# Kernel optimization log

Hardware: AMD Instinct MI355X
Metric: run time of the kernel (lower is better)

## Reference

```python
import jax, jax.numpy as jnp
import numpy as np

B, N, F_IN = 4, 8000, 3          # batch, electrons per event, (x,y,z) features
HID, S, T = 128, 1024, 1024      # MLP hidden, n_sensors, waveform_ticks
INV_SQRT_2PI = 0.3989422804


def _mlp(x, W1, b1, W2, b2):
    h = jax.nn.relu(x @ W1 + b1)
    return h @ W2 + b2


def setup_inputs() -> dict:
    key = jax.random.key(0)
    ks = jax.random.split(key, 12)
    simulator_input = jax.random.normal(ks[0], (B, N, F_IN), dtype=jnp.float32)
    # z positions in tick units, spread across the waveform
    z_positions = jax.random.uniform(ks[1], (B, N), dtype=jnp.float32) * (T - 1)
    mask = jnp.ones((B, N, 1), dtype=jnp.float32)
    s1 = 1.0 / np.sqrt(F_IN)
    s2 = 1.0 / np.sqrt(HID)
    Wp1 = jax.random.normal(ks[2], (F_IN, HID), dtype=jnp.float32) * s1
    bp1 = jnp.zeros((HID,), dtype=jnp.float32)
    Wp2 = jax.random.normal(ks[3], (HID, S), dtype=jnp.float32) * s2
    bp2 = jnp.zeros((S,), dtype=jnp.float32)
    Wa1 = jax.random.normal(ks[4], (F_IN, HID), dtype=jnp.float32) * s1
    ba1 = jnp.zeros((HID,), dtype=jnp.float32)
    Wa2 = jax.random.normal(ks[5], (HID, S), dtype=jnp.float32) * s2
    ba2 = jnp.zeros((S,), dtype=jnp.float32)
    nn_bin_sigma = 5.0 * jnp.ones((1,), dtype=jnp.float32)  # self.variable init
    return dict(simulator_input=simulator_input, z_positions=z_positions, mask=mask,
                Wp1=Wp1, bp1=bp1, Wp2=Wp2, bp2=bp2,
                Wa1=Wa1, ba1=ba1, Wa2=Wa2, ba2=ba2,
                nn_bin_sigma=nn_bin_sigma)


def reference(simulator_input, z_positions, mask,
              Wp1, bp1, Wp2, bp2, Wa1, ba1, Wa2, ba2, nn_bin_sigma):
    # sensor response per electron: sigmoid(prob MLP) * amp MLP * mask  -> [B,N,S]
    sensor_probs = jax.nn.sigmoid(_mlp(simulator_input, Wp1, bp1, Wp2, bp2))
    el_light_amp = _mlp(simulator_input, Wa1, ba1, Wa2, ba2)
    response_of_sensors = el_light_amp * sensor_probs * mask

    # Gaussian binning kernel over waveform ticks: [B,N,T]
    ticks = jnp.arange(T, dtype=simulator_input.dtype)          # linspace(0, T-1, T)
    sigma = nn_bin_sigma[0]
    diff = ticks[None, None, :] - z_positions[:, :, None]
    exp_values = jnp.exp(-(diff ** 2) / (2.0 * sigma ** 2)) * (INV_SQRT_2PI / jnp.sqrt(sigma ** 2))

    # per-batch waveforms = sensor_response.T @ exp_values -> [B,S,T]; then sum over batch
    waveforms = jnp.einsum('bns,bnt->st', response_of_sensors, exp_values)
    return waveforms  # [S, T]
```

## Files before the change

### kernel.cpp

```cpp
#include <hip/hip_runtime.h>


#define BN_E   32000
#define NBLK   125
#define HIDW   128
#define S_DIM  1024
#define T_DIM  1024
#define NBKT   16
#define KSPL   4
#define MAXPAD (BN_E + NBKT * 31)
#define MAXCG  ((MAXPAD + 31) / 32)
#define INV_SQRT_2PI 0.3989422804f

typedef __attribute__((ext_vector_type(8))) unsigned short u16x8;
typedef __attribute__((ext_vector_type(8))) __bf16         bf16x8;
typedef __attribute__((ext_vector_type(4))) float          f32x4;

static __device__ __forceinline__ unsigned short f2bf(float f) {
    union { float f; unsigned int u; } v; v.f = f;
    unsigned int r = v.u + 0x7FFFu + ((v.u >> 16) & 1u);
    return (unsigned short)(r >> 16);
}

static __device__ __forceinline__ f32x4 mfma16(u16x8 a, u16x8 b, f32x4 c) {
    return __builtin_amdgcn_mfma_f32_16x16x32_bf16(
        __builtin_bit_cast(bf16x8, a), __builtin_bit_cast(bf16x8, b), c, 0, 0, 0);
}

static __device__ __forceinline__ int bucket_of(float z) {
    int b = (int)floorf((z - 31.f) * (1.f / 64.f));
    return min(max(b, 0), NBKT - 1);
}

__global__ __launch_bounds__(256) void k_count(const float* __restrict__ z,
                                               int* __restrict__ bc,
                                               float* __restrict__ out) {
    int bx = blockIdx.x;
    if (bx >= NBLK) {
        int idx = (bx - NBLK) * 256 + threadIdx.x;
        ((f32x4*)out)[idx] = (f32x4){0.f, 0.f, 0.f, 0.f};
        return;
    }
    __shared__ int h[NBKT];
    if (threadIdx.x < NBKT) h[threadIdx.x] = 0;
    __syncthreads();
    int e = bx * 256 + threadIdx.x;
    atomicAdd(&h[bucket_of(z[e])], 1);
    __syncthreads();
    if (threadIdx.x < NBKT) bc[bx * NBKT + threadIdx.x] = h[threadIdx.x];
}

__global__ __launch_bounds__(256) void k_fillscan(const float* __restrict__ z,
                                                  const int* __restrict__ bc,
                                                  int* __restrict__ meta,
                                                  int* __restrict__ list) {
    __shared__ int part[16][16];
    __shared__ int segoff[16][16];
    __shared__ int cntL[NBKT], pstartL[NBKT], baseL[NBKT], h[NBKT];
    int t = threadIdx.x, b = t & 15, seg = t >> 4;
    int v[8]; int sum = 0;
#pragma unroll
    for (int i = 0; i < 8; ++i) {
        int blk = seg * 8 + i;
        v[i] = (blk < NBLK) ? bc[blk * NBKT + b] : 0;
        sum += v[i];
    }
    part[seg][b] = sum;
    if (t < NBKT) h[t] = 0;
    __syncthreads();
    if (t < NBKT) {
        int run = 0;
        for (int s = 0; s < 16; ++s) { segoff[s][t] = run; run += part[s][t]; }
        cntL[t] = run;
    }
    __syncthreads();
    if (t == 0) {
        int s = 0;
        for (int i = 0; i < NBKT; ++i) {
            pstartL[i] = s;
            s += ((cntL[i] + 31) >> 5) << 5;
        }
        if (blockIdx.x == 0) {
            for (int i = 0; i < NBKT; ++i) { meta[i] = cntL[i]; meta[32 + i] = pstartL[i]; }
            meta[48] = s;
        }
    }
    __syncthreads();
    if (t < NBKT) {
        int me = blockIdx.x;
        int run = segoff[me >> 3][t];
        for (int k = 0; k < (me & 7); ++k)
            run += bc[((me >> 3) * 8 + k) * NBKT + t];
        baseL[t] = pstartL[t] + run;
    }
    __syncthreads();
    int e = blockIdx.x * 256 + t;
    int b2 = bucket_of(z[e]);
    int r = atomicAdd(&h[b2], 1);
    list[baseL[b2] + r] = e;
}

__global__ __launch_bounds__(256) void k_prep(
    const float* __restrict__ x, const float* __restrict__ zg,
    const float* __restrict__ maskg, const float* __restrict__ sigp,
    const float* __restrict__ Wp1, const float* __restrict__ bp1,
    const float* __restrict__ Wa1, const float* __restrict__ ba1,
    const float* __restrict__ Wp2, const float* __restrict__ Wa2,
    const int* __restrict__ meta, const int* __restrict__ list,
    unsigned short* __restrict__ HpS, unsigned short* __restrict__ HaS,
    unsigned short* __restrict__ GT,
    unsigned short* __restrict__ WfP, unsigned short* __restrict__ WfA) {
    int bx = blockIdx.x;
    if (bx < MAXCG) {
        int tid = threadIdx.x;

        __shared__ float W1L[1024];
        __shared__ float zzL[32], cmL[32];
        __shared__ int metaL[33];
        if (tid < 33) metaL[tid] = meta[tid < 16 ? tid : (tid < 32 ? tid + 16 : 48)];
        if (tid < 96)                        ((float4*)W1L)[tid]              = ((const float4*)Wp1)[tid];
        else if (tid < 128)                  ((float4*)(W1L + 384))[tid - 96] = ((const float4*)bp1)[tid - 96];
        else if (tid < 224)                  ((float4*)(W1L + 512))[tid - 128]= ((const float4*)Wa1)[tid - 128];
        else                                 ((float4*)(W1L + 896))[tid - 224]= ((const float4*)ba1)[tid - 224];
        __syncthreads();

        int pos0 = bx * 32;
        if (pos0 >= metaL[32]) return;
        int b = 15;
        while (metaL[16 + b] > pos0) --b;
        int tb = b * 64, cnt = metaL[b], pstart = metaL[16 + b];

        if (tid < 32) {
            int pos = pos0 + tid;
            bool real = (pos - pstart) < cnt;
            int ev = real ? list[pos] : 0;
            float sigma = sigp[0];
            zzL[tid] = real ? zg[ev] : 0.f;
            cmL[tid] = real ? (INV_SQRT_2PI / sigma) * maskg[ev] : 0.f;
        }

        {
            int e_l = tid & 31, part = tid >> 5;
            int pos = pos0 + e_l;
            bool real = (pos - pstart) < cnt;
            int ev = real ? list[pos] : 0;
            float x0 = 0.f, x1 = 0.f, x2 = 0.f;
            if (real) { x0 = x[ev * 3]; x1 = x[ev * 3 + 1]; x2 = x[ev * 3 + 2]; }
            unsigned short hp[16], ha[16];
#pragma unroll
            for (int i = 0; i < 16; ++i) {
                int j = part * 16 + i;
                float hv = x0 * W1L[j] + x1 * W1L[128 + j] + x2 * W1L[256 + j] + W1L[384 + j];
                float av = x0 * W1L[512 + j] + x1 * W1L[640 + j] + x2 * W1L[768 + j] + W1L[896 + j];
                hp[i] = real ? f2bf(fmaxf(hv, 0.f)) : (unsigned short)0;
                ha[i] = real ? f2bf(fmaxf(av, 0.f)) : (unsigned short)0;
            }
#pragma unroll
            for (int h2 = 0; h2 < 2; ++h2) {
                int u = (2 * part + h2) * 32 + e_l;
                *(uint4*)&HpS[(size_t)bx * 4096 + u * 8] = ((uint4*)hp)[h2];
                *(uint4*)&HaS[(size_t)bx * 4096 + u * 8] = ((uint4*)ha)[h2];
            }
        }
        __syncthreads();

        {
            float sigma = sigp[0];
            float nis2 = -1.f / (2.f * sigma * sigma);
#pragma unroll
            for (int uu = 0; uu < 2; ++uu) {
                int u = tid * 2 + uu;
                int n8 = u >> 6, q = (u >> 4) & 3, c = u & 15;
                float tt = (float)(tb + n8 * 16 + c);
                unsigned short g8[8];
#pragma unroll
                for (int j = 0; j < 8; ++j) {
                    int e = q * 8 + j;
                    float d = tt - zzL[e];
                    g8[j] = f2bf(cmL[e] * __expf(d * d * nis2));
                }
                *(uint4*)&GT[(size_t)bx * 4096 + u * 8] = *(uint4*)g8;
            }
        }
    } else {
        int bid = bx - MAXCG;
        const float* src = (bid & 64) ? Wa2 : Wp2;
        unsigned short* dst = (bid & 64) ? WfA : WfP;
        int rem = bid & 63;
        int kq = rem >> 2;
        int s  = (rem & 3) * 256 + threadIdx.x;
        int ks = kq >> 2, q = kq & 3;
        unsigned short fr[8];
#pragma unroll
        for (int j = 0; j < 8; ++j)
            fr[j] = f2bf(src[(ks * 32 + q * 8 + j) * S_DIM + s]);
        ((u16x8*)dst)[kq * S_DIM + s] = *(u16x8*)fr;
    }
}

__global__ __launch_bounds__(512, 4) void k_main(
    const unsigned short* __restrict__ HpS, const unsigned short* __restrict__ HaS,
    const unsigned short* __restrict__ WfP, const unsigned short* __restrict__ WfA,
    const float* __restrict__ bp2, const float* __restrict__ ba2,
    const int* __restrict__ meta, const unsigned short* __restrict__ GT,
    float* __restrict__ out) {

    const int bk     = blockIdx.x / KSPL;
    const int kspl   = blockIdx.x % KSPL;
    const int s0     = blockIdx.y * 128;
    const int tb     = bk * 64;
    const int cnt    = meta[bk];
    const int pstart = meta[32 + bk];
    const int nch    = (cnt + 31) >> 5;
    const int per    = (nch + KSPL - 1) / KSPL;
    const int c0     = kspl * per;
    const int c1     = min(nch, c0 + per);
    if (c0 >= c1) return;

    const int tid = threadIdx.x;
    const int w = tid >> 6, l = tid & 63, q = l >> 4, c = l & 15;

    __shared__ __align__(16) uint4 HpL[1024];
    __shared__ __align__(16) uint4 HaL[1024];
    __shared__ __align__(16) unsigned short RspL[128 * 40];

    const u16x8* WfPv = (const u16x8*)WfP;
    const u16x8* WfAv = (const u16x8*)WfA;
    const int sg = s0 + w * 16 + c;
    u16x8 wP[4], wA[4];
#pragma unroll
    for (int ks = 0; ks < 4; ++ks) {
        wP[ks] = WfPv[(ks * 4 + q) * S_DIM + sg];
        wA[ks] = WfAv[(ks * 4 + q) * S_DIM + sg];
    }
    const float bp2v = bp2[sg];
    const float ba2v = ba2[sg];

    const f32x4 z4 = { 0.f, 0.f, 0.f, 0.f };
    f32x4 acc2[8];
#pragma unroll
    for (int n8 = 0; n8 < 8; ++n8) acc2[n8] = z4;

    const uint4* Hp4 = (const uint4*)HpS;
    const uint4* Ha4 = (const uint4*)HaS;
    const int cgBase = pstart >> 5;

    size_t cb = (size_t)(cgBase + c0) * 512;
    uint4 p = Hp4[cb + tid];
    uint4 a = Ha4[cb + tid];

    for (int ci = c0; ci < c1; ++ci) {
        const int buf = ((ci - c0) & 1) << 9;
        HpL[buf + tid] = p;
        HaL[buf + tid] = a;

        int nc = min(ci + 1, c1 - 1);
        cb = (size_t)(cgBase + nc) * 512;
        p = Hp4[cb + tid];
        a = Ha4[cb + tid];
        __syncthreads();

        const unsigned short* gt = GT + (size_t)(cgBase + ci) * 4096;
        u16x8 bfr[8];
#pragma unroll
        for (int n8 = 0; n8 < 8; ++n8)
            bfr[n8] = *(const u16x8*)&gt[((n8 * 4 + q) * 16 + c) * 8];

        const u16x8* StHp = (const u16x8*)(HpL + buf);
        const u16x8* StHa = (const u16x8*)(HaL + buf);
        f32x4 aP[2], aA[2];
        aP[0] = z4; aP[1] = z4; aA[0] = z4; aA[1] = z4;
#pragma unroll
        for (int ks = 0; ks < 4; ++ks) {
            u16x8 hp0 = StHp[(ks * 4 + q) * 32 + c];
            u16x8 hp1 = StHp[(ks * 4 + q) * 32 + c + 16];
            u16x8 ha0 = StHa[(ks * 4 + q) * 32 + c];
            u16x8 ha1 = StHa[(ks * 4 + q) * 32 + c + 16];
            aP[0] = mfma16(hp0, wP[ks], aP[0]);
            aP[1] = mfma16(hp1, wP[ks], aP[1]);
            aA[0] = mfma16(ha0, wA[ks], aA[0]);
            aA[1] = mfma16(ha1, wA[ks], aA[1]);
        }

#pragma unroll
        for (int m = 0; m < 2; ++m) {
            f32x4 pp = aP[m], aa = aA[m];
            unsigned long long pk = 0;
#pragma unroll
            for (int r = 0; r < 4; ++r) {
                float pr = pp[r] + bp2v;
                float ar = aa[r] + ba2v;
                float sg2 = __builtin_amdgcn_rcpf(1.f + __expf(-pr));
                pk |= (unsigned long long)f2bf(sg2 * ar) << (16 * r);
            }
            *(unsigned long long*)&RspL[(w * 16 + c) * 40 + m * 16 + q * 4] = pk;
        }

        u16x8 afr = *(const u16x8*)&RspL[(w * 16 + c) * 40 + q * 8];
#pragma unroll
        for (int n8 = 0; n8 < 8; ++n8)
            acc2[n8] = mfma16(afr, bfr[n8], acc2[n8]);
    }

#pragma unroll
    for (int n8 = 0; n8 < 8; ++n8) {
        int t = tb + n8 * 16 + c;
        if (t < T_DIM) {
            int srow = s0 + w * 16 + q * 4;
#pragma unroll
            for (int r = 0; r < 4; ++r)
                atomicAdd(&out[(srow + r) * T_DIM + t], acc2[n8][r]);
        }
    }
}


extern "C" void kernel_launch(void* const* d_in, const int* in_sizes, int n_in,
                              void* d_out, int out_size, void* d_ws, size_t ws_size,
                              hipStream_t stream) {
    const float* x    = (const float*)d_in[0];
    const float* zp   = (const float*)d_in[1];
    const float* mask = (const float*)d_in[2];
    const float* Wp1  = (const float*)d_in[3];
    const float* bp1  = (const float*)d_in[4];
    const float* Wp2  = (const float*)d_in[5];
    const float* bp2  = (const float*)d_in[6];
    const float* Wa1  = (const float*)d_in[7];
    const float* ba1  = (const float*)d_in[8];
    const float* Wa2  = (const float*)d_in[9];
    const float* ba2  = (const float*)d_in[10];
    const float* sig  = (const float*)d_in[11];

    char* ws = (char*)d_ws;
    unsigned short* HpS  = (unsigned short*)(ws);
    unsigned short* HaS  = (unsigned short*)(ws + 8323072);
    unsigned short* WfP  = (unsigned short*)(ws + 16646144);
    unsigned short* WfA  = (unsigned short*)(ws + 16908288);
    int*            meta = (int*)(ws + 17170432);
    int*            list = (int*)(ws + 17170688);
    int*            bc   = (int*)(ws + 17300736);
    unsigned short* GT   = (unsigned short*)(ws + 17308736);

    k_count<<<NBLK + 1024, 256, 0, stream>>>(zp, bc, (float*)d_out);
    k_fillscan<<<NBLK, 256, 0, stream>>>(zp, bc, meta, list);
    k_prep<<<MAXCG + 128, 256, 0, stream>>>(x, zp, mask, sig,
                                            Wp1, bp1, Wa1, ba1, Wp2, Wa2,
                                            meta, list, HpS, HaS, GT, WfP, WfA);
    k_main<<<dim3(NBKT * KSPL, 8, 1), 512, 0, stream>>>(
        HpS, HaS, WfP, WfA, bp2, ba2, meta, GT, (float*)d_out);
}
```

Measured before the change: 148.7 us.

## Replace output atomics with per-block partial buffers and a deterministic reduce kernel

The main kernel no longer atomically adds its 128x128 tile (64 ticks of own bucket plus overlap into the next bucket) into the output. Each block instead writes its tile to a private partial buffer in workspace, zeroing it when the block has no work. A new reduce kernel sums the KSPL split partials and the overlapping neighbour bucket per output element. This removes atomic contention and the separate output-zeroing pass. In exchange it adds an extra kernel launch and roughly 16 MB of partial-buffer traffic.

```diff
diff --git a/kernel.cpp b/kernel.cpp
--- a/kernel.cpp
+++ b/kernel.cpp
@@ -33,14 +33,8 @@
 }
 
 __global__ __launch_bounds__(256) void k_count(const float* __restrict__ z,
-                                               int* __restrict__ bc,
-                                               float* __restrict__ out) {
+                                               int* __restrict__ bc) {
     int bx = blockIdx.x;
-    if (bx >= NBLK) {
-        int idx = (bx - NBLK) * 256 + threadIdx.x;
-        ((f32x4*)out)[idx] = (f32x4){0.f, 0.f, 0.f, 0.f};
-        return;
-    }
     __shared__ int h[NBKT];
     if (threadIdx.x < NBKT) h[threadIdx.x] = 0;
     __syncthreads();
@@ -203,22 +197,29 @@
     const unsigned short* __restrict__ WfP, const unsigned short* __restrict__ WfA,
     const float* __restrict__ bp2, const float* __restrict__ ba2,
     const int* __restrict__ meta, const unsigned short* __restrict__ GT,
-    float* __restrict__ out) {
+    float* __restrict__ P) {
 
     const int bk     = blockIdx.x / KSPL;
     const int kspl   = blockIdx.x % KSPL;
     const int s0     = blockIdx.y * 128;
-    const int tb     = bk * 64;
     const int cnt    = meta[bk];
     const int pstart = meta[32 + bk];
     const int nch    = (cnt + 31) >> 5;
     const int per    = (nch + KSPL - 1) / KSPL;
     const int c0     = kspl * per;
     const int c1     = min(nch, c0 + per);
-    if (c0 >= c1) return;
 
     const int tid = threadIdx.x;
     const int w = tid >> 6, l = tid & 63, q = l >> 4, c = l & 15;
+    const f32x4 z4 = { 0.f, 0.f, 0.f, 0.f };
+    float* Pp = P + (size_t)(blockIdx.x * 8 + blockIdx.y) * 16384;
+
+    if (c0 >= c1) {
+        f32x4* p4 = (f32x4*)Pp;
+#pragma unroll
+        for (int i = 0; i < 8; ++i) p4[i * 512 + tid] = z4;
+        return;
+    }
 
     __shared__ __align__(16) uint4 HpL[1024];
     __shared__ __align__(16) uint4 HaL[1024];
@@ -236,7 +237,6 @@
     const float bp2v = bp2[sg];
     const float ba2v = ba2[sg];
 
-    const f32x4 z4 = { 0.f, 0.f, 0.f, 0.f };
     f32x4 acc2[8];
 #pragma unroll
     for (int n8 = 0; n8 < 8; ++n8) acc2[n8] = z4;
@@ -304,14 +304,39 @@
 
 #pragma unroll
     for (int n8 = 0; n8 < 8; ++n8) {
-        int t = tb + n8 * 16 + c;
-        if (t < T_DIM) {
-            int srow = s0 + w * 16 + q * 4;
-#pragma unroll
-            for (int r = 0; r < 4; ++r)
-                atomicAdd(&out[(srow + r) * T_DIM + t], acc2[n8][r]);
-        }
-    }
+        int tl = n8 * 16 + c;
+        int sl = w * 16 + q * 4;
+#pragma unroll
+        for (int r = 0; r < 4; ++r)
+            Pp[(sl + r) * 128 + tl] = acc2[n8][r];
+    }
+}
+
+__global__ __launch_bounds__(256) void k_reduce(const float* __restrict__ P,
+                                                float* __restrict__ out) {
+    int idx = blockIdx.x * 256 + threadIdx.x;
+    int t0  = (idx & 255) << 2;
+    int s   = idx >> 8;
+    int bkA = t0 >> 6;
+    int colA = t0 & 63;
+    int y    = s >> 7;
+    int sl   = s & 127;
+    const f32x4* P4 = (const f32x4*)P;
+    f32x4 acc = { 0.f, 0.f, 0.f, 0.f };
+#pragma unroll
+    for (int k = 0; k < KSPL; ++k) {
+        f32x4 v = P4[((size_t)(bkA * KSPL + k) * 8 + y) * 4096 + sl * 32 + (colA >> 2)];
+        acc[0] += v[0]; acc[1] += v[1]; acc[2] += v[2]; acc[3] += v[3];
+    }
+    if (bkA > 0) {
+        int colB = 64 + colA;
+#pragma unroll
+        for (int k = 0; k < KSPL; ++k) {
+            f32x4 v = P4[((size_t)((bkA - 1) * KSPL + k) * 8 + y) * 4096 + sl * 32 + (colB >> 2)];
+            acc[0] += v[0]; acc[1] += v[1]; acc[2] += v[2]; acc[3] += v[3];
+        }
+    }
+    ((f32x4*)out)[idx] = acc;
 }
 
 
@@ -340,12 +365,14 @@
     int*            list = (int*)(ws + 17170688);
     int*            bc   = (int*)(ws + 17300736);
     unsigned short* GT   = (unsigned short*)(ws + 17308736);
-
-    k_count<<<NBLK + 1024, 256, 0, stream>>>(zp, bc, (float*)d_out);
+    float*          P    = (float*)(ws + 25631808);
+
+    k_count<<<NBLK, 256, 0, stream>>>(zp, bc);
     k_fillscan<<<NBLK, 256, 0, stream>>>(zp, bc, meta, list);
     k_prep<<<MAXCG + 128, 256, 0, stream>>>(x, zp, mask, sig,
                                             Wp1, bp1, Wa1, ba1, Wp2, Wa2,
                                             meta, list, HpS, HaS, GT, WfP, WfA);
     k_main<<<dim3(NBKT * KSPL, 8, 1), 512, 0, stream>>>(
-        HpS, HaS, WfP, WfA, bp2, ba2, meta, GT, (float*)d_out);
-}
+        HpS, HaS, WfP, WfA, bp2, ba2, meta, GT, P);
+    k_reduce<<<1024, 256, 0, stream>>>(P, (float*)d_out);
+}
```

Measured after the change: 145.0 us. 1.03x faster.
